# Optimization experiments

Hardware: AMD Instinct MI355X
Metric: run time of the kernel (lower is better)

Reference implementation:

```python
import jax, jax.numpy as jnp
import numpy as np
import math

B, T, D, H = 4, 1024, 1024, 16
DK = D // H
TAU_THRESH = 0.3


def setup_inputs() -> dict:
    key = jax.random.key(0)
    ks = jax.random.split(key, 13)
    s = 1.0 / math.sqrt(D)
    return {
        "x": jax.random.normal(ks[0], (B, T, D), dtype=jnp.float32),
        "Wq": jax.random.normal(ks[1], (D, D), dtype=jnp.float32) * s,
        "bq": jax.random.normal(ks[2], (D,), dtype=jnp.float32) * s,
        "Wk": jax.random.normal(ks[3], (D, D), dtype=jnp.float32) * s,
        "bk": jax.random.normal(ks[4], (D,), dtype=jnp.float32) * s,
        "Wv": jax.random.normal(ks[5], (D, D), dtype=jnp.float32) * s,
        "bv": jax.random.normal(ks[6], (D,), dtype=jnp.float32) * s,
        "Wo": jax.random.normal(ks[7], (D, D), dtype=jnp.float32) * s,
        "bo": jax.random.normal(ks[8], (D,), dtype=jnp.float32) * s,
        "Wg1": jax.random.normal(ks[9], (1, D), dtype=jnp.float32) * s,
        "bg1": jax.random.normal(ks[10], (1,), dtype=jnp.float32) * s,
        "Wg2": jax.random.normal(ks[11], (1, D), dtype=jnp.float32) * s,
        "bg2": jax.random.normal(ks[12], (1,), dtype=jnp.float32) * s,
    }


def reference(x, Wq, bq, Wk, bk, Wv, bv, Wo, bo, Wg1, bg1, Wg2, bg2):
    b, t, d = x.shape
    # projections (torch Linear: y = x @ W.T + b)
    Q = (x @ Wq.T + bq).reshape(b, t, H, DK).transpose(0, 2, 1, 3)  # [B,H,T,dk]
    K = (x @ Wk.T + bk).reshape(b, t, H, DK).transpose(0, 2, 1, 3)
    V = (x @ Wv.T + bv).reshape(b, t, H, DK).transpose(0, 2, 1, 3)
    scores = jnp.einsum("bhqd,bhkd->bhqk", Q, K) / math.sqrt(DK)  # [B,H,T,T]
    # confidence gates from first-token query context [B, H*dk] = [B, D]
    context = Q[:, :, 0, :].reshape(b, d)
    q1 = jax.nn.sigmoid(context @ Wg1.T + bg1)  # [B,1]
    q2 = jax.nn.sigmoid(context @ Wg2.T + bg2)  # [B,1]
    c = jnp.clip(q1 * q2, 1e-8, 1.0)            # [B,1]
    tau = jnp.where(c < TAU_THRESH, 1.0 / c, jnp.ones_like(c)).reshape(b, 1, 1, 1)
    p = jax.nn.softmax(scores / tau, axis=-1)
    cb = c.reshape(b, 1, 1, 1)
    p_gated = cb * p + (1.0 - cb) * (1.0 / t)
    u = jnp.mean(1.0 - c, axis=-1, keepdims=True)  # [B,1]
    attn_out = jnp.einsum("bhqk,bhkd->bhqd", p_gated, V)
    attn_out = attn_out.transpose(0, 2, 1, 3).reshape(b, t, d)
    output = attn_out @ Wo.T + bo
    return output, u
```

## Files before the change

kernel.cpp:

```cpp
#include <hip/hip_runtime.h>
#include <stdint.h>

typedef short bf16x8 __attribute__((ext_vector_type(8)));
typedef float f32x4 __attribute__((ext_vector_type(4)));

#define MFMA_BF16(a, b, c) __builtin_amdgcn_mfma_f32_16x16x32_bf16((a), (b), (c), 0, 0, 0)

__device__ __forceinline__ short f2bf(float x) {
  union { float f; uint32_t u; } v; v.f = x;
  uint32_t r = (v.u + 0x7FFFu + ((v.u >> 16) & 1u)) >> 16;
  return (short)r;
}
__device__ __forceinline__ uint32_t rnd_bf_hi(float x) {
  union { float f; uint32_t u; } v; v.f = x;
  return v.u + 0x7FFFu + ((v.u >> 16) & 1u);
}
__device__ __forceinline__ uint32_t pack2bf(float a, float b) {
  return __builtin_amdgcn_perm(rnd_bf_hi(b), rnd_bf_hi(a), 0x07060302);
}
__device__ __forceinline__ float bfbits2f(uint32_t b16) {
  union { uint32_t u; float f; } v; v.u = b16 << 16; return v.f;
}
__device__ __forceinline__ float fexp2(float x) {
#if __has_builtin(__builtin_amdgcn_exp2f)
  return __builtin_amdgcn_exp2f(x);
#else
  return __expf(x * 0.6931471805599453f);
#endif
}
__device__ __forceinline__ void async16(const void* g, void* l) {
  __builtin_amdgcn_global_load_lds(
      (const __attribute__((address_space(1))) uint32_t*)g,
      (__attribute__((address_space(3))) uint32_t*)l, 16, 0, 0);
}

__global__ __launch_bounds__(256) void cvt_bf16_k(const float* __restrict__ in,
                                                  short* __restrict__ out, int n4) {
  int i = blockIdx.x * 256 + threadIdx.x;
  if (i < n4) {
    float4 v = ((const float4*)in)[i];
    short4 o;
    o.x = f2bf(v.x); o.y = f2bf(v.y); o.z = f2bf(v.z); o.w = f2bf(v.w);
    ((short4*)out)[i] = o;
  }
}

__global__ __launch_bounds__(256) void gates_ctx(const float* __restrict__ x,
                                                 const float* __restrict__ Wq,
                                                 const float* __restrict__ bq,
                                                 float* __restrict__ ctx) {
  const int b = blockIdx.x;
  const int n0 = blockIdx.y << 6;
  __shared__ float xs[1024];
  const int tid = threadIdx.x;
  for (int i = tid; i < 1024; i += 256) xs[i] = x[b * 1048576 + i];
  __syncthreads();
  const int w = tid >> 6, lane = tid & 63;
  const float4* xv4 = (const float4*)xs;
  for (int rr = 0; rr < 16; ++rr) {
    const int n = n0 + (w << 4) + rr;
    const float4* wrow = (const float4*)(Wq + n * 1024);
    float p = 0.f;
#pragma unroll
    for (int c2 = 0; c2 < 4; ++c2) {
      float4 wv = wrow[lane + (c2 << 6)];
      float4 xv = xv4[lane + (c2 << 6)];
      p += xv.x * wv.x + xv.y * wv.y + xv.z * wv.z + xv.w * wv.w;
    }
#pragma unroll
    for (int off = 32; off; off >>= 1) p += __shfl_xor(p, off);
    if (lane == 0) ctx[b * 1024 + n] = p + bq[n];
  }
}

__global__ __launch_bounds__(256) void gates_fin(const float* __restrict__ ctx,
                                                 const float* __restrict__ Wg1,
                                                 const float* __restrict__ bg1,
                                                 const float* __restrict__ Wg2,
                                                 const float* __restrict__ bg2,
                                                 float* __restrict__ gates,
                                                 float* __restrict__ u_out) {
  __shared__ float red[16];
  const int tid = threadIdx.x, w = tid >> 6, lane = tid & 63;
  for (int b = 0; b < 4; ++b) {
    float4 cv = ((const float4*)(ctx + b * 1024))[tid];
    float4 w1 = ((const float4*)Wg1)[tid];
    float4 w2 = ((const float4*)Wg2)[tid];
    float p1 = cv.x * w1.x + cv.y * w1.y + cv.z * w1.z + cv.w * w1.w;
    float p2 = cv.x * w2.x + cv.y * w2.y + cv.z * w2.z + cv.w * w2.w;
#pragma unroll
    for (int off = 32; off; off >>= 1) { p1 += __shfl_xor(p1, off); p2 += __shfl_xor(p2, off); }
    if (lane == 0) { red[w] = p1; red[8 + w] = p2; }
    __syncthreads();
    if (tid == 0) {
      float g1 = red[0] + red[1] + red[2] + red[3] + bg1[0];
      float g2 = red[8] + red[9] + red[10] + red[11] + bg2[0];
      float q1 = 1.f / (1.f + expf(-g1));
      float q2 = 1.f / (1.f + expf(-g2));
      float c = fminf(fmaxf(q1 * q2, 1e-8f), 1.0f);
      gates[b * 2 + 0] = c;
      gates[b * 2 + 1] = (c < 0.3f ? c : 1.0f) * 0.125f;
      u_out[b] = 1.0f - c;
    }
    __syncthreads();
  }
}

__global__ __launch_bounds__(256) void gemm_qkv(
    const short* __restrict__ xb,
    const short* __restrict__ Wqb, const short* __restrict__ Wkb, const short* __restrict__ Wvb,
    const float* __restrict__ bq, const float* __restrict__ bk, const float* __restrict__ bv,
    const float* __restrict__ gat,
    short* __restrict__ Qh, short* __restrict__ Kh, short* __restrict__ Vt) {
  const int z = blockIdx.z;
  const short* W = (z == 0) ? Wqb : (z == 1) ? Wkb : Wvb;
  const float* bias = (z == 0) ? bq : (z == 1) ? bk : bv;

  const int m0 = blockIdx.x << 7;
  const int n0 = blockIdx.y << 7;
  const int tid = threadIdx.x;
  const int w = tid >> 6, lane = tid & 63;
  const int m15 = lane & 15, quad = lane >> 4;
  const int wr = w >> 1, wc = w & 1;

  const float qsc = (z == 0) ? gat[(m0 >> 10) * 2 + 1] * 1.4426950408889634f : 1.0f;

  __shared__ short As[128 * 32];
  __shared__ short Bs[128 * 32];

  f32x4 acc[4][4];
#pragma unroll
  for (int i = 0; i < 4; ++i)
#pragma unroll
    for (int j = 0; j < 4; ++j) { f32x4 zz = {0.f, 0.f, 0.f, 0.f}; acc[i][j] = zz; }

  const int srow = (w << 5) + (lane >> 2);
  const int scol = (lane & 3) << 3;
  const short* ga0 = xb + (m0 + srow) * 1024 + scol;
  const short* ga1 = ga0 + 16 * 1024;
  const short* gb0 = W + (n0 + srow) * 1024 + scol;
  const short* gb1 = gb0 + 16 * 1024;
  short* la0 = &As[srow * 32 + scol];
  short* la1 = la0 + 512;
  short* lb0 = &Bs[srow * 32 + scol];
  short* lb1 = lb0 + 512;

  for (int kt = 0; kt < 32; ++kt) {
    async16(ga0, la0); async16(ga1, la1);
    async16(gb0, lb0); async16(gb1, lb1);
    ga0 += 32; ga1 += 32; gb0 += 32; gb1 += 32;
    __syncthreads();
    bf16x8 a[4], b[4];
#pragma unroll
    for (int i = 0; i < 4; ++i)
      a[i] = *(const bf16x8*)(&As[((wr << 6) + (i << 4) + m15) * 32 + (quad << 3)]);
#pragma unroll
    for (int j = 0; j < 4; ++j)
      b[j] = *(const bf16x8*)(&Bs[((wc << 6) + (j << 4) + m15) * 32 + (quad << 3)]);
#pragma unroll
    for (int i = 0; i < 4; ++i)
#pragma unroll
      for (int j = 0; j < 4; ++j)
        acc[i][j] = MFMA_BF16(a[i], b[j], acc[i][j]);
    __syncthreads();
  }

#pragma unroll
  for (int j = 0; j < 4; ++j) {
    const int n = n0 + (wc << 6) + (j << 4) + m15;
    const float bb_ = bias[n];
    const int h = n >> 6, dk = n & 63;
#pragma unroll
    for (int i = 0; i < 4; ++i) {
      const int mb = m0 + (wr << 6) + (i << 4) + (quad << 2);
#pragma unroll
      for (int r = 0; r < 4; ++r) {
        const int m = mb + r;
        const int batch = m >> 10, t = m & 1023;
        const short o = f2bf((acc[i][j][r] + bb_) * qsc);
        if (z == 2) {
          Vt[((batch * 16 + h) * 64 + dk) * 1024 + t] = o;
        } else if (z == 1) {
          Kh[((batch * 16 + h) * 1024 + t) * 64 + dk] = o;
        } else {
          Qh[((batch * 16 + h) * 1024 + t) * 64 + dk] = o;
        }
      }
    }
  }
}

__global__ __launch_bounds__(256) void gemm_out(const short* __restrict__ Ab,
                                                const short* __restrict__ Wo,
                                                const float* __restrict__ bo,
                                                float* __restrict__ Cout) {
  const int m0 = blockIdx.x << 7;
  const int n0 = blockIdx.y << 7;
  const int tid = threadIdx.x;
  const int w = tid >> 6, lane = tid & 63;
  const int m15 = lane & 15, quad = lane >> 4;
  const int wr = w >> 1, wc = w & 1;

  __shared__ short As[128 * 32];
  __shared__ short Bs[128 * 32];

  f32x4 acc[4][4];
#pragma unroll
  for (int i = 0; i < 4; ++i)
#pragma unroll
    for (int j = 0; j < 4; ++j) { f32x4 zz = {0.f, 0.f, 0.f, 0.f}; acc[i][j] = zz; }

  const int srow = (w << 5) + (lane >> 2);
  const int scol = (lane & 3) << 3;
  const short* ga0 = Ab + (m0 + srow) * 1024 + scol;
  const short* ga1 = ga0 + 16 * 1024;
  const short* gb0 = Wo + (n0 + srow) * 1024 + scol;
  const short* gb1 = gb0 + 16 * 1024;
  short* la0 = &As[srow * 32 + scol];
  short* la1 = la0 + 512;
  short* lb0 = &Bs[srow * 32 + scol];
  short* lb1 = lb0 + 512;

  for (int kt = 0; kt < 32; ++kt) {
    async16(ga0, la0); async16(ga1, la1);
    async16(gb0, lb0); async16(gb1, lb1);
    ga0 += 32; ga1 += 32; gb0 += 32; gb1 += 32;
    __syncthreads();
    bf16x8 a[4], b[4];
#pragma unroll
    for (int i = 0; i < 4; ++i)
      a[i] = *(const bf16x8*)(&As[((wr << 6) + (i << 4) + m15) * 32 + (quad << 3)]);
#pragma unroll
    for (int j = 0; j < 4; ++j)
      b[j] = *(const bf16x8*)(&Bs[((wc << 6) + (j << 4) + m15) * 32 + (quad << 3)]);
#pragma unroll
    for (int i = 0; i < 4; ++i)
#pragma unroll
      for (int j = 0; j < 4; ++j)
        acc[i][j] = MFMA_BF16(a[i], b[j], acc[i][j]);
    __syncthreads();
  }

#pragma unroll
  for (int j = 0; j < 4; ++j) {
    const int n = n0 + (wc << 6) + (j << 4) + m15;
    const float bb_ = bo[n];
#pragma unroll
    for (int i = 0; i < 4; ++i) {
      const int mb = m0 + (wr << 6) + (i << 4) + (quad << 2);
#pragma unroll
      for (int r = 0; r < 4; ++r)
        Cout[(mb + r) * 1024 + n] = acc[i][j][r] + bb_;
    }
  }
}

__global__ __launch_bounds__(256) void meanv_k(const short* __restrict__ Vt,
                                               float* __restrict__ meanV) {
  const int bh = blockIdx.x;
  const int tid = threadIdx.x;
  const int d = tid >> 2, part = tid & 3;
  const short* row = Vt + bh * 65536 + d * 1024 + part * 256;
  float s = 0.f;
#pragma unroll 4
  for (int i = 0; i < 64; ++i) {
    uint2 v = *(const uint2*)(row + i * 4);
    s += bfbits2f(v.x & 0xffffu) + bfbits2f(v.x >> 16) +
         bfbits2f(v.y & 0xffffu) + bfbits2f(v.y >> 16);
  }
  s += __shfl_xor(s, 1);
  s += __shfl_xor(s, 2);
  if (part == 0) meanV[bh * 64 + d] = s * (1.0f / 1024.0f);
}

__global__ __launch_bounds__(256, 4) void attn_k(const short* __restrict__ Qh,
                                                 const short* __restrict__ Kh,
                                                 const short* __restrict__ Vt,
                                                 const float* __restrict__ gates,
                                                 const float* __restrict__ meanV,
                                                 short* __restrict__ attnb) {
  const int bh = blockIdx.x;
  const int b = bh >> 4, h = bh & 15;
  const int q0 = blockIdx.y << 6;
  const int tid = threadIdx.x;
  const int w = tid >> 6, lane = tid & 63;
  const int m15 = lane & 15, quad = lane >> 4;

  __shared__ short Ks[2][4096];
  __shared__ short Vs[2][4096];

  const short* ksrc = Kh + bh * 65536;
  const short* vsrc = Vt + bh * 65536;

  const short* qsrc = Qh + ((bh << 10) + q0 + (w << 4) + m15) * 64;
  const bf16x8 qb0 = *(const bf16x8*)(qsrc + (quad << 3));
  const bf16x8 qb1 = *(const bf16x8*)(qsrc + 32 + (quad << 3));

  const int off0 = tid, off1 = tid + 256;
  const int r0 = off0 >> 3, cb0 = (off0 & 7) ^ (r0 & 7);
  const int r1 = off1 >> 3, cb1 = (off1 & 7) ^ (r1 & 7);

#define STAGE(kv, bufi)                                                        \
  do {                                                                         \
    async16(ksrc + (((kv) << 6) + r0) * 64 + (cb0 << 3), &Ks[bufi][off0 << 3]);\
    async16(ksrc + (((kv) << 6) + r1) * 64 + (cb1 << 3), &Ks[bufi][off1 << 3]);\
    async16(vsrc + r0 * 1024 + ((kv) << 6) + (cb0 << 3), &Vs[bufi][off0 << 3]);\
    async16(vsrc + r1 * 1024 + ((kv) << 6) + (cb1 << 3), &Vs[bufi][off1 << 3]);\
  } while (0)

  STAGE(0, 0);

  float lsum = 0.f;
  f32x4 o_acc[4];
#pragma unroll
  for (int jd = 0; jd < 4; ++jd) { f32x4 zz = {0.f, 0.f, 0.f, 0.f}; o_acc[jd] = zz; }

  const int srcA = ((quad & 1) << 5) + m15;
  const int srcB = srcA + 16;
  const bool selhi = (quad & 2) != 0;

  for (int kv = 0; kv < 16; ++kv) {
    __syncthreads();
    if (kv < 15) STAGE(kv + 1, (kv + 1) & 1);
    const short* Kb = &Ks[kv & 1][0];
    const short* Vb = &Vs[kv & 1][0];

    f32x4 sacc[4];
#pragma unroll
    for (int s = 0; s < 4; ++s) {
      const int row = (s << 4) + m15;
      const int sw = row & 7;
      bf16x8 a0 = *(const bf16x8*)(Kb + (row << 6) + ((quad ^ sw) << 3));
      bf16x8 a1 = *(const bf16x8*)(Kb + (row << 6) + (((quad + 4) ^ sw) << 3));
      f32x4 zz = {0.f, 0.f, 0.f, 0.f};
      zz = MFMA_BF16(a0, qb0, zz);
      zz = MFMA_BF16(a1, qb1, zz);
      sacc[s] = zz;
    }

    uint32_t pk[4][2];
#pragma unroll
    for (int s = 0; s < 4; ++s) {
      float p0 = fexp2(sacc[s][0]);
      float p1 = fexp2(sacc[s][1]);
      float p2 = fexp2(sacc[s][2]);
      float p3 = fexp2(sacc[s][3]);
      lsum += (p0 + p1) + (p2 + p3);
      pk[s][0] = pack2bf(p0, p1);
      pk[s][1] = pack2bf(p2, p3);
    }

    bf16x8 pf[2];
#pragma unroll
    for (int H = 0; H < 2; ++H) {
      uint32_t f[4];
#pragma unroll
      for (int rp = 0; rp < 2; ++rp) {
        uint32_t alo = (uint32_t)__shfl((int)pk[2 * H][rp], srcA);
        uint32_t ahi = (uint32_t)__shfl((int)pk[2 * H + 1][rp], srcA);
        uint32_t blo = (uint32_t)__shfl((int)pk[2 * H][rp], srcB);
        uint32_t bhi = (uint32_t)__shfl((int)pk[2 * H + 1][rp], srcB);
        f[rp]     = selhi ? ahi : alo;
        f[2 + rp] = selhi ? bhi : blo;
      }
      pf[H] = *(bf16x8*)f;
    }

#pragma unroll
    for (int jd = 0; jd < 4; ++jd) {
      const int row = (jd << 4) + m15;
      const int sw = row & 7;
      bf16x8 v0 = *(const bf16x8*)(Vb + (row << 6) + ((quad ^ sw) << 3));
      bf16x8 v1 = *(const bf16x8*)(Vb + (row << 6) + (((quad + 4) ^ sw) << 3));
      o_acc[jd] = MFMA_BF16(v0, pf[0], o_acc[jd]);
      o_acc[jd] = MFMA_BF16(v1, pf[1], o_acc[jd]);
    }
  }
#undef STAGE

  float l = lsum;
  l += __shfl_xor(l, 16);
  l += __shfl_xor(l, 32);

  const float cg = gates[b * 2 + 0];
  const float s0 = cg / l;
  const float omc = 1.0f - cg;
  const int qrow = q0 + (w << 4) + m15;
  short* orow = attnb + ((b << 10) + qrow) * 1024 + (h << 6);
#pragma unroll
  for (int jd = 0; jd < 4; ++jd) {
    float4 mv = *(const float4*)(meanV + (bh << 6) + (jd << 4) + (quad << 2));
    float v0_ = s0 * o_acc[jd][0] + omc * mv.x;
    float v1_ = s0 * o_acc[jd][1] + omc * mv.y;
    float v2_ = s0 * o_acc[jd][2] + omc * mv.z;
    float v3_ = s0 * o_acc[jd][3] + omc * mv.w;
    uint2 st;
    st.x = pack2bf(v0_, v1_);
    st.y = pack2bf(v2_, v3_);
    *(uint2*)(orow + (jd << 4) + (quad << 2)) = st;
  }
}

extern "C" void kernel_launch(void* const* d_in, const int* in_sizes, int n_in,
                              void* d_out, int out_size, void* d_ws, size_t ws_size,
                              hipStream_t stream) {
  const float* x   = (const float*)d_in[0];
  const float* Wq  = (const float*)d_in[1];
  const float* bq  = (const float*)d_in[2];
  const float* Wk  = (const float*)d_in[3];
  const float* bk  = (const float*)d_in[4];
  const float* Wv  = (const float*)d_in[5];
  const float* bv  = (const float*)d_in[6];
  const float* Wo  = (const float*)d_in[7];
  const float* bo  = (const float*)d_in[8];
  const float* Wg1 = (const float*)d_in[9];
  const float* bg1 = (const float*)d_in[10];
  const float* Wg2 = (const float*)d_in[11];
  const float* bg2 = (const float*)d_in[12];
  float* out = (float*)d_out;

  char* ws = (char*)d_ws;
  short* xb   = (short*)(ws + 0);
  short* Wqb  = (short*)(ws + 8388608);
  short* Wkb  = (short*)(ws + 10485760);
  short* Wvb  = (short*)(ws + 12582912);
  short* Wob  = (short*)(ws + 14680064);
  short* Qh   = (short*)(ws + 16777216);
  short* Kh   = (short*)(ws + 25165824);
  short* Vt   = (short*)(ws + 33554432);
  short* attb = (short*)(ws + 41943040);
  float* ctx  = (float*)(ws + 50331648);
  float* gat  = (float*)(ws + 50348032);
  float* mV   = (float*)(ws + 50348064);

  cvt_bf16_k<<<4096, 256, 0, stream>>>(x,  xb,  1048576);
  cvt_bf16_k<<<1024, 256, 0, stream>>>(Wq, Wqb, 262144);
  cvt_bf16_k<<<1024, 256, 0, stream>>>(Wk, Wkb, 262144);
  cvt_bf16_k<<<1024, 256, 0, stream>>>(Wv, Wvb, 262144);
  cvt_bf16_k<<<1024, 256, 0, stream>>>(Wo, Wob, 262144);

  gates_ctx<<<dim3(4, 16), 256, 0, stream>>>(x, Wq, bq, ctx);
  gates_fin<<<1, 256, 0, stream>>>(ctx, Wg1, bg1, Wg2, bg2, gat, out + 4194304);

  gemm_qkv<<<dim3(32, 8, 3), 256, 0, stream>>>(xb, Wqb, Wkb, Wvb, bq, bk, bv, gat, Qh, Kh, Vt);
  meanv_k<<<64, 256, 0, stream>>>(Vt, mV);
  attn_k<<<dim3(64, 16), 256, 0, stream>>>(Qh, Kh, Vt, gat, mV, attb);
  gemm_out<<<dim3(32, 8), 256, 0, stream>>>(attb, Wob, bo, out);
}
```

Baseline: 223.9 us.

## Double-buffer GEMM tiles, fuse conversions, transpose V via LDS, shrink out-proj tile

The five fp32-to-bf16 conversion launches are merged into one kernel. Both GEMMs now double-buffer their LDS tiles so the next K-slice loads while the current one computes, with one barrier per iteration instead of two. The V epilogue stages through a swizzled LDS tile and writes 16-byte coalesced rows of Vt instead of scattered 2-byte stores. The output projection uses 64x128 tiles to double the block count, trading per-block reuse for better CU occupancy.

```diff
diff --git a/kernel.cpp b/kernel.cpp
--- a/kernel.cpp
+++ b/kernel.cpp
@@ -34,15 +34,27 @@
       (__attribute__((address_space(3))) uint32_t*)l, 16, 0, 0);
 }
 
-__global__ __launch_bounds__(256) void cvt_bf16_k(const float* __restrict__ in,
-                                                  short* __restrict__ out, int n4) {
-  int i = blockIdx.x * 256 + threadIdx.x;
-  if (i < n4) {
-    float4 v = ((const float4*)in)[i];
-    short4 o;
-    o.x = f2bf(v.x); o.y = f2bf(v.y); o.z = f2bf(v.z); o.w = f2bf(v.w);
-    ((short4*)out)[i] = o;
-  }
+__global__ __launch_bounds__(256) void cvt_all(
+    const float* __restrict__ x, const float* __restrict__ Wq,
+    const float* __restrict__ Wk, const float* __restrict__ Wv,
+    const float* __restrict__ Wo,
+    short* __restrict__ xb, short* __restrict__ Wqb, short* __restrict__ Wkb,
+    short* __restrict__ Wvb, short* __restrict__ Wob) {
+  const int bid = blockIdx.x;
+  const float* src; short* dst; int idx;
+  if (bid < 4096) {
+    src = x; dst = xb; idx = (bid << 8) + threadIdx.x;
+  } else {
+    const int r = bid - 4096;
+    const int z = r >> 10;
+    src = (z == 0) ? Wq : (z == 1) ? Wk : (z == 2) ? Wv : Wo;
+    dst = (z == 0) ? Wqb : (z == 1) ? Wkb : (z == 2) ? Wvb : Wob;
+    idx = ((r & 1023) << 8) + threadIdx.x;
+  }
+  float4 v = ((const float4*)src)[idx];
+  short4 o;
+  o.x = f2bf(v.x); o.y = f2bf(v.y); o.z = f2bf(v.z); o.w = f2bf(v.w);
+  ((short4*)dst)[idx] = o;
 }
 
 __global__ __launch_bounds__(256) void gates_ctx(const float* __restrict__ x,
@@ -125,8 +137,8 @@
 
   const float qsc = (z == 0) ? gat[(m0 >> 10) * 2 + 1] * 1.4426950408889634f : 1.0f;
 
-  __shared__ short As[128 * 32];
-  __shared__ short Bs[128 * 32];
+  __shared__ short As[2][4096];
+  __shared__ short Bs[2][4096];
 
   f32x4 acc[4][4];
 #pragma unroll
@@ -136,54 +148,83 @@
 
   const int srow = (w << 5) + (lane >> 2);
   const int scol = (lane & 3) << 3;
-  const short* ga0 = xb + (m0 + srow) * 1024 + scol;
-  const short* ga1 = ga0 + 16 * 1024;
-  const short* gb0 = W + (n0 + srow) * 1024 + scol;
-  const short* gb1 = gb0 + 16 * 1024;
-  short* la0 = &As[srow * 32 + scol];
-  short* la1 = la0 + 512;
-  short* lb0 = &Bs[srow * 32 + scol];
-  short* lb1 = lb0 + 512;
-
+  const int l0 = srow * 32 + scol;
+  const short* gA = xb + (m0 + srow) * 1024 + scol;
+  const short* gB = W + (n0 + srow) * 1024 + scol;
+
+#define GSTAGE(kt, bi)                                              \
+  do {                                                              \
+    const short* A_ = gA + ((kt) << 5);                             \
+    const short* B_ = gB + ((kt) << 5);                             \
+    async16(A_, &As[bi][l0]); async16(A_ + 16384, &As[bi][l0 + 512]);\
+    async16(B_, &Bs[bi][l0]); async16(B_ + 16384, &Bs[bi][l0 + 512]);\
+  } while (0)
+
+  GSTAGE(0, 0);
   for (int kt = 0; kt < 32; ++kt) {
-    async16(ga0, la0); async16(ga1, la1);
-    async16(gb0, lb0); async16(gb1, lb1);
-    ga0 += 32; ga1 += 32; gb0 += 32; gb1 += 32;
-    __syncthreads();
+    __syncthreads();
+    if (kt < 31) GSTAGE(kt + 1, (kt + 1) & 1);
+    const int cur = kt & 1;
     bf16x8 a[4], b[4];
 #pragma unroll
     for (int i = 0; i < 4; ++i)
-      a[i] = *(const bf16x8*)(&As[((wr << 6) + (i << 4) + m15) * 32 + (quad << 3)]);
+      a[i] = *(const bf16x8*)(&As[cur][((wr << 6) + (i << 4) + m15) * 32 + (quad << 3)]);
 #pragma unroll
     for (int j = 0; j < 4; ++j)
-      b[j] = *(const bf16x8*)(&Bs[((wc << 6) + (j << 4) + m15) * 32 + (quad << 3)]);
+      b[j] = *(const bf16x8*)(&Bs[cur][((wc << 6) + (j << 4) + m15) * 32 + (quad << 3)]);
 #pragma unroll
     for (int i = 0; i < 4; ++i)
 #pragma unroll
       for (int j = 0; j < 4; ++j)
         acc[i][j] = MFMA_BF16(a[i], b[j], acc[i][j]);
-    __syncthreads();
-  }
-
-#pragma unroll
-  for (int j = 0; j < 4; ++j) {
-    const int n = n0 + (wc << 6) + (j << 4) + m15;
-    const float bb_ = bias[n];
-    const int h = n >> 6, dk = n & 63;
-#pragma unroll
-    for (int i = 0; i < 4; ++i) {
-      const int mb = m0 + (wr << 6) + (i << 4) + (quad << 2);
-#pragma unroll
-      for (int r = 0; r < 4; ++r) {
-        const int m = mb + r;
-        const int batch = m >> 10, t = m & 1023;
-        const short o = f2bf((acc[i][j][r] + bb_) * qsc);
-        if (z == 2) {
-          Vt[((batch * 16 + h) * 64 + dk) * 1024 + t] = o;
-        } else if (z == 1) {
-          Kh[((batch * 16 + h) * 1024 + t) * 64 + dk] = o;
-        } else {
-          Qh[((batch * 16 + h) * 1024 + t) * 64 + dk] = o;
+  }
+#undef GSTAGE
+
+  if (z == 2) {
+    __syncthreads();
+    short* Ts = (w < 2) ? &As[w][0] : &Bs[w - 2][0];
+    const int batch = m0 >> 10;
+    const int tb0 = (m0 & 1023) + (wr << 6);
+    const int h = (n0 >> 6) + wc;
+#pragma unroll
+    for (int j = 0; j < 4; ++j) {
+      const int dkl = (j << 4) + m15;
+      const float bb_ = bias[n0 + (wc << 6) + dkl];
+#pragma unroll
+      for (int i = 0; i < 4; ++i) {
+        uint2 pk;
+        pk.x = pack2bf(acc[i][j][0] + bb_, acc[i][j][1] + bb_);
+        pk.y = pack2bf(acc[i][j][2] + bb_, acc[i][j][3] + bb_);
+        const int blk = (i << 1) + (quad >> 1);
+        const int addr = (dkl << 6) + ((blk ^ (dkl & 7)) << 3) + ((quad & 1) << 2);
+        *(uint2*)&Ts[addr] = pk;
+      }
+    }
+    __syncthreads();
+    const int tb = lane & 7, dr = lane >> 3;
+#pragma unroll
+    for (int it = 0; it < 8; ++it) {
+      const int dkl = dr + (it << 3);
+      const int addr = (dkl << 6) + ((tb ^ (dkl & 7)) << 3);
+      uint4 vv = *(const uint4*)&Ts[addr];
+      *(uint4*)(Vt + ((((batch << 4) + h) << 6) + dkl) * 1024 + tb0 + (tb << 3)) = vv;
+    }
+  } else {
+#pragma unroll
+    for (int j = 0; j < 4; ++j) {
+      const int n = n0 + (wc << 6) + (j << 4) + m15;
+      const float bb_ = bias[n];
+      const int h = n >> 6, dk = n & 63;
+#pragma unroll
+      for (int i = 0; i < 4; ++i) {
+        const int mb = m0 + (wr << 6) + (i << 4) + (quad << 2);
+#pragma unroll
+        for (int r = 0; r < 4; ++r) {
+          const int m = mb + r;
+          const int batch = m >> 10, t = m & 1023;
+          const short o = f2bf((acc[i][j][r] + bb_) * qsc);
+          if (z == 1) Kh[((batch * 16 + h) * 1024 + t) * 64 + dk] = o;
+          else        Qh[((batch * 16 + h) * 1024 + t) * 64 + dk] = o;
         }
       }
     }
@@ -194,60 +235,67 @@
                                                 const short* __restrict__ Wo,
                                                 const float* __restrict__ bo,
                                                 float* __restrict__ Cout) {
-  const int m0 = blockIdx.x << 7;
+  const int m0 = blockIdx.x << 6;
   const int n0 = blockIdx.y << 7;
   const int tid = threadIdx.x;
   const int w = tid >> 6, lane = tid & 63;
   const int m15 = lane & 15, quad = lane >> 4;
   const int wr = w >> 1, wc = w & 1;
 
-  __shared__ short As[128 * 32];
-  __shared__ short Bs[128 * 32];
-
-  f32x4 acc[4][4];
-#pragma unroll
-  for (int i = 0; i < 4; ++i)
+  __shared__ short As[2][2048];
+  __shared__ short Bs[2][4096];
+
+  f32x4 acc[2][4];
+#pragma unroll
+  for (int i = 0; i < 2; ++i)
 #pragma unroll
     for (int j = 0; j < 4; ++j) { f32x4 zz = {0.f, 0.f, 0.f, 0.f}; acc[i][j] = zz; }
+
+  const int arow = tid >> 2;
+  const int acol = (tid & 3) << 3;
+  const int lA = arow * 32 + acol;
+  const short* gA = Ab + (m0 + arow) * 1024 + acol;
 
   const int srow = (w << 5) + (lane >> 2);
   const int scol = (lane & 3) << 3;
-  const short* ga0 = Ab + (m0 + srow) * 1024 + scol;
-  const short* ga1 = ga0 + 16 * 1024;
-  const short* gb0 = Wo + (n0 + srow) * 1024 + scol;
-  const short* gb1 = gb0 + 16 * 1024;
-  short* la0 = &As[srow * 32 + scol];
-  short* la1 = la0 + 512;
-  short* lb0 = &Bs[srow * 32 + scol];
-  short* lb1 = lb0 + 512;
-
+  const int lB = srow * 32 + scol;
+  const short* gB = Wo + (n0 + srow) * 1024 + scol;
+
+#define OSTAGE(kt, bi)                                              \
+  do {                                                              \
+    const short* A_ = gA + ((kt) << 5);                             \
+    const short* B_ = gB + ((kt) << 5);                             \
+    async16(A_, &As[bi][lA]);                                       \
+    async16(B_, &Bs[bi][lB]); async16(B_ + 16384, &Bs[bi][lB + 512]);\
+  } while (0)
+
+  OSTAGE(0, 0);
   for (int kt = 0; kt < 32; ++kt) {
-    async16(ga0, la0); async16(ga1, la1);
-    async16(gb0, lb0); async16(gb1, lb1);
-    ga0 += 32; ga1 += 32; gb0 += 32; gb1 += 32;
-    __syncthreads();
-    bf16x8 a[4], b[4];
-#pragma unroll
-    for (int i = 0; i < 4; ++i)
-      a[i] = *(const bf16x8*)(&As[((wr << 6) + (i << 4) + m15) * 32 + (quad << 3)]);
+    __syncthreads();
+    if (kt < 31) OSTAGE(kt + 1, (kt + 1) & 1);
+    const int cur = kt & 1;
+    bf16x8 a[2], b[4];
+#pragma unroll
+    for (int i = 0; i < 2; ++i)
+      a[i] = *(const bf16x8*)(&As[cur][((wr << 5) + (i << 4) + m15) * 32 + (quad << 3)]);
 #pragma unroll
     for (int j = 0; j < 4; ++j)
-      b[j] = *(const bf16x8*)(&Bs[((wc << 6) + (j << 4) + m15) * 32 + (quad << 3)]);
-#pragma unroll
-    for (int i = 0; i < 4; ++i)
+      b[j] = *(const bf16x8*)(&Bs[cur][((wc << 6) + (j << 4) + m15) * 32 + (quad << 3)]);
+#pragma unroll
+    for (int i = 0; i < 2; ++i)
 #pragma unroll
       for (int j = 0; j < 4; ++j)
         acc[i][j] = MFMA_BF16(a[i], b[j], acc[i][j]);
-    __syncthreads();
-  }
+  }
+#undef OSTAGE
 
 #pragma unroll
   for (int j = 0; j < 4; ++j) {
     const int n = n0 + (wc << 6) + (j << 4) + m15;
     const float bb_ = bo[n];
 #pragma unroll
-    for (int i = 0; i < 4; ++i) {
-      const int mb = m0 + (wr << 6) + (i << 4) + (quad << 2);
+    for (int i = 0; i < 2; ++i) {
+      const int mb = m0 + (wr << 5) + (i << 4) + (quad << 2);
 #pragma unroll
       for (int r = 0; r < 4; ++r)
         Cout[(mb + r) * 1024 + n] = acc[i][j][r] + bb_;
@@ -433,11 +481,7 @@
   float* gat  = (float*)(ws + 50348032);
   float* mV   = (float*)(ws + 50348064);
 
-  cvt_bf16_k<<<4096, 256, 0, stream>>>(x,  xb,  1048576);
-  cvt_bf16_k<<<1024, 256, 0, stream>>>(Wq, Wqb, 262144);
-  cvt_bf16_k<<<1024, 256, 0, stream>>>(Wk, Wkb, 262144);
-  cvt_bf16_k<<<1024, 256, 0, stream>>>(Wv, Wvb, 262144);
-  cvt_bf16_k<<<1024, 256, 0, stream>>>(Wo, Wob, 262144);
+  cvt_all<<<8192, 256, 0, stream>>>(x, Wq, Wk, Wv, Wo, xb, Wqb, Wkb, Wvb, Wob);
 
   gates_ctx<<<dim3(4, 16), 256, 0, stream>>>(x, Wq, bq, ctx);
   gates_fin<<<1, 256, 0, stream>>>(ctx, Wg1, bg1, Wg2, bg2, gat, out + 4194304);
@@ -445,5 +489,5 @@
   gemm_qkv<<<dim3(32, 8, 3), 256, 0, stream>>>(xb, Wqb, Wkb, Wvb, bq, bk, bv, gat, Qh, Kh, Vt);
   meanv_k<<<64, 256, 0, stream>>>(Vt, mV);
   attn_k<<<dim3(64, 16), 256, 0, stream>>>(Qh, Kh, Vt, gat, mV, attb);
-  gemm_out<<<dim3(32, 8), 256, 0, stream>>>(attb, Wob, bo, out);
-}
+  gemm_out<<<dim3(64, 8), 256, 0, stream>>>(attb, Wob, bo, out);
+}
```

Result: no change. 227.7 us (+1.7%).
